# Kernel optimization log

Measured on AMD Instinct MI355X. Metric: run time of the kernel, lower is better.

## Reference

```python
import jax, jax.numpy as jnp
import numpy as np

K_SIZE = 3
STRIDE = 1
PAD = 1


def _extract_patches(X, k, stride, pad):
    """X: [N,H,W,C] -> patches [N,Ho,Wo,k*k*C], ordered (dh, dw, c) to match
    filters.reshape(c_out, k*k*C)."""
    Xp = jnp.pad(X, ((0, 0), (pad, pad), (pad, pad), (0, 0)))
    N, Hp, Wp, C = Xp.shape
    Ho = (Hp - k) // stride + 1
    Wo = (Wp - k) // stride + 1
    slabs = [Xp[:, dh:dh + stride * Ho:stride, dw:dw + stride * Wo:stride, :]
             for dh in range(k) for dw in range(k)]  # fixed small k*k loop
    P = jnp.stack(slabs, axis=3)  # [N,Ho,Wo,k*k,C]
    return P.reshape(N, Ho, Wo, k * k * C)


def setup_inputs() -> dict:
    key = jax.random.key(0)
    k1, k2 = jax.random.split(key)
    X = jax.random.normal(k1, (8, 32, 32, 32), dtype=jnp.float32)
    filters = jax.random.normal(k2, (64, 3, 3, 32), dtype=jnp.float32)
    return {"X": X, "filters": filters}


def reference(X, filters):
    # AdderNet forward: Z[n,h,w,f] = sum_{dh,dw,c} |window(n,h,w) - filters[f]|
    c_out = filters.shape[0]
    P = _extract_patches(X, K_SIZE, STRIDE, PAD)  # [N,Ho,Wo,K]
    N, Ho, Wo, K = P.shape
    F = filters.reshape(c_out, K)
    # L1 distance between every patch and every filter: [M, c_out]
    D = jnp.abs(P.reshape(-1, 1, K) - F[None, :, :]).sum(axis=-1)
    return D.reshape(N, Ho, Wo, c_out)
```

## Files before the change

### kernel.cpp

```cpp
#include <hip/hip_runtime.h>


#define BLOCK 256

__global__ __launch_bounds__(256, 2) void adder_fwd(const float* __restrict__ X,
                                                    const float* __restrict__ Fg,
                                                    float* __restrict__ out) {
    __shared__ float Xs[4 * 34 * 36];

    const int b = blockIdx.x;
    const int fq = b & 3;
    const int hp = (b >> 2) & 15;
    const int n = b >> 6;
    const int h0 = hp * 2;
    const int tid = threadIdx.x;

    #pragma unroll
    for (int i = 0; i < 5; ++i) {
        int idx = tid + BLOCK * i;
        if (idx < 1088) {
            int c4 = idx & 7;
            int t  = idx >> 3;
            int wc = t % 34;
            int rr = t / 34;
            int hr = h0 + rr - 1;
            int gw = wc - 1;
            float4 v = make_float4(0.f, 0.f, 0.f, 0.f);
            if ((unsigned)hr < 32u && (unsigned)gw < 32u) {
                v = ((const float4*)(X + (((size_t)n * 32 + hr) * 32 + gw) * 32))[c4];
            }
            ((float4*)(Xs + (rr * 34 + wc) * 36))[c4] = v;
        }
    }
    __syncthreads();

    const int w    = tid & 31;
    const int hh   = (tid >> 5) & 1;
    const int wave = __builtin_amdgcn_readfirstlane(tid >> 6);
    const int f0   = fq * 16 + wave * 4;

    const float* fb = Fg + (size_t)f0 * 288;

    float a0 = 0.f, a1 = 0.f, a2 = 0.f, a3 = 0.f;

    #pragma unroll
    for (int r = 0; r < 3; ++r) {
        #pragma unroll
        for (int dw = 0; dw < 3; ++dw) {
            const float4* xp = (const float4*)(Xs + ((hh + r) * 34 + (w + dw)) * 36);
            const float*  ftap = fb + (r * 3 + dw) * 32;
            #pragma unroll
            for (int c4 = 0; c4 < 8; ++c4) {
                float4 xv = xp[c4];
                float4 f0v = ((const float4*)(ftap + 0 * 288))[c4];
                float4 f1v = ((const float4*)(ftap + 1 * 288))[c4];
                float4 f2v = ((const float4*)(ftap + 2 * 288))[c4];
                float4 f3v = ((const float4*)(ftap + 3 * 288))[c4];
                a0 += fabsf(xv.x - f0v.x) + fabsf(xv.y - f0v.y)
                    + fabsf(xv.z - f0v.z) + fabsf(xv.w - f0v.w);
                a1 += fabsf(xv.x - f1v.x) + fabsf(xv.y - f1v.y)
                    + fabsf(xv.z - f1v.z) + fabsf(xv.w - f1v.w);
                a2 += fabsf(xv.x - f2v.x) + fabsf(xv.y - f2v.y)
                    + fabsf(xv.z - f2v.z) + fabsf(xv.w - f2v.w);
                a3 += fabsf(xv.x - f3v.x) + fabsf(xv.y - f3v.y)
                    + fabsf(xv.z - f3v.z) + fabsf(xv.w - f3v.w);
            }
        }
    }

    float4* o4 = (float4*)out;
    o4[(((size_t)n * 32 + h0 + hh) * 32 + w) * 16 + (f0 >> 2)] =
        make_float4(a0, a1, a2, a3);
}

extern "C" void kernel_launch(void* const* d_in, const int* in_sizes, int n_in,
                              void* d_out, int out_size, void* d_ws, size_t ws_size,
                              hipStream_t stream) {
    const float* X = (const float*)d_in[0];
    const float* F = (const float*)d_in[1];
    float* out = (float*)d_out;
    adder_fwd<<<dim3(512), dim3(256), 0, stream>>>(X, F, out);
}
```

Measured before the change: 69.17 us.

## Keep filters in registers, split channels across lanes, and reuse LDS input windows

```diff
diff --git a/kernel.cpp b/kernel.cpp
--- a/kernel.cpp
+++ b/kernel.cpp
@@ -3,74 +3,103 @@
 
 #define BLOCK 256
 
-__global__ __launch_bounds__(256, 2) void adder_fwd(const float* __restrict__ X,
+__global__ __launch_bounds__(256, 4) void adder_fwd(const float* __restrict__ X,
                                                     const float* __restrict__ Fg,
                                                     float* __restrict__ out) {
-    __shared__ float Xs[4 * 34 * 36];
+    __shared__ float Xs[3 * 18 * 32];
 
-    const int b = blockIdx.x;
-    const int fq = b & 3;
-    const int hp = (b >> 2) & 15;
-    const int n = b >> 6;
-    const int h0 = hp * 2;
+    const int b  = blockIdx.x;
+    const int fh = b & 1;
+    const int wh = (b >> 1) & 1;
+    const int h  = (b >> 2) & 31;
+    const int n  = b >> 7;
+    const int w0 = wh * 16;
     const int tid = threadIdx.x;
 
+    const int lane = tid & 63;
+    const int c8   = lane & 7;
+    const int f    = lane >> 3;
+    const int wave = __builtin_amdgcn_readfirstlane(tid >> 6);
+    const int f0   = fh * 32 + wave * 8;
+    const int fid  = f0 + f;
+
+    float4 fr[9];
+    {
+        const float* fp = Fg + (size_t)fid * 288 + c8 * 4;
+        #pragma unroll
+        for (int t = 0; t < 9; ++t)
+            fr[t] = *(const float4*)(fp + t * 32);
+    }
+
     #pragma unroll
-    for (int i = 0; i < 5; ++i) {
-        int idx = tid + BLOCK * i;
-        if (idx < 1088) {
-            int c4 = idx & 7;
-            int t  = idx >> 3;
-            int wc = t % 34;
-            int rr = t / 34;
-            int hr = h0 + rr - 1;
-            int gw = wc - 1;
+    for (int it = 0; it < 2; ++it) {
+        int idx = tid + BLOCK * it;
+        if (idx < 432) {
+            int c4  = idx & 7;
+            int t   = idx >> 3;
+            int col = t % 18;
+            int row = t / 18;
+            int hr  = h + row - 1;
+            int gw  = w0 + col - 1;
             float4 v = make_float4(0.f, 0.f, 0.f, 0.f);
-            if ((unsigned)hr < 32u && (unsigned)gw < 32u) {
+            if ((unsigned)hr < 32u && (unsigned)gw < 32u)
                 v = ((const float4*)(X + (((size_t)n * 32 + hr) * 32 + gw) * 32))[c4];
-            }
-            ((float4*)(Xs + (rr * 34 + wc) * 36))[c4] = v;
+            ((float4*)(Xs + (row * 18 + col) * 32))[c4] = v;
         }
     }
     __syncthreads();
 
-    const int w    = tid & 31;
-    const int hh   = (tid >> 5) & 1;
-    const int wave = __builtin_amdgcn_readfirstlane(tid >> 6);
-    const int f0   = fq * 16 + wave * 4;
+    const float* xb = Xs + c8 * 4;
+    const size_t obase = (((size_t)n * 32 + h) * 32 + w0) * 64 + fid;
 
-    const float* fb = Fg + (size_t)f0 * 288;
+    #pragma unroll 1
+    for (int pg = 0; pg < 4; ++pg) {
+        float4 acc[4];
+        #pragma unroll
+        for (int pp = 0; pp < 4; ++pp)
+            acc[pp] = make_float4(0.f, 0.f, 0.f, 0.f);
 
-    float a0 = 0.f, a1 = 0.f, a2 = 0.f, a3 = 0.f;
+        #pragma unroll
+        for (int dh = 0; dh < 3; ++dh) {
+            float4 x[6];
+            #pragma unroll
+            for (int j = 0; j < 6; ++j)
+                x[j] = *(const float4*)(xb + (dh * 18 + pg * 4 + j) * 32);
 
-    #pragma unroll
-    for (int r = 0; r < 3; ++r) {
-        #pragma unroll
-        for (int dw = 0; dw < 3; ++dw) {
-            const float4* xp = (const float4*)(Xs + ((hh + r) * 34 + (w + dw)) * 36);
-            const float*  ftap = fb + (r * 3 + dw) * 32;
             #pragma unroll
-            for (int c4 = 0; c4 < 8; ++c4) {
-                float4 xv = xp[c4];
-                float4 f0v = ((const float4*)(ftap + 0 * 288))[c4];
-                float4 f1v = ((const float4*)(ftap + 1 * 288))[c4];
-                float4 f2v = ((const float4*)(ftap + 2 * 288))[c4];
-                float4 f3v = ((const float4*)(ftap + 3 * 288))[c4];
-                a0 += fabsf(xv.x - f0v.x) + fabsf(xv.y - f0v.y)
-                    + fabsf(xv.z - f0v.z) + fabsf(xv.w - f0v.w);
-                a1 += fabsf(xv.x - f1v.x) + fabsf(xv.y - f1v.y)
-                    + fabsf(xv.z - f1v.z) + fabsf(xv.w - f1v.w);
-                a2 += fabsf(xv.x - f2v.x) + fabsf(xv.y - f2v.y)
-                    + fabsf(xv.z - f2v.z) + fabsf(xv.w - f2v.w);
-                a3 += fabsf(xv.x - f3v.x) + fabsf(xv.y - f3v.y)
-                    + fabsf(xv.z - f3v.z) + fabsf(xv.w - f3v.w);
+            for (int dw = 0; dw < 3; ++dw) {
+                const float4 fv = fr[dh * 3 + dw];
+                #pragma unroll
+                for (int pp = 0; pp < 4; ++pp) {
+                    const float4 xv = x[pp + dw];
+                    acc[pp].x += fabsf(xv.x - fv.x);
+                    acc[pp].y += fabsf(xv.y - fv.y);
+                    acc[pp].z += fabsf(xv.z - fv.z);
+                    acc[pp].w += fabsf(xv.w - fv.w);
+                }
             }
         }
+
+        float s0 = (acc[0].x + acc[0].y) + (acc[0].z + acc[0].w);
+        float s1 = (acc[1].x + acc[1].y) + (acc[1].z + acc[1].w);
+        float s2 = (acc[2].x + acc[2].y) + (acc[2].z + acc[2].w);
+        float s3 = (acc[3].x + acc[3].y) + (acc[3].z + acc[3].w);
+
+        s0 += __shfl_xor(s0, 1, 64);  s1 += __shfl_xor(s1, 1, 64);
+        s2 += __shfl_xor(s2, 1, 64);  s3 += __shfl_xor(s3, 1, 64);
+        s0 += __shfl_xor(s0, 2, 64);  s1 += __shfl_xor(s1, 2, 64);
+        s2 += __shfl_xor(s2, 2, 64);  s3 += __shfl_xor(s3, 2, 64);
+        s0 += __shfl_xor(s0, 4, 64);  s1 += __shfl_xor(s1, 4, 64);
+        s2 += __shfl_xor(s2, 4, 64);  s3 += __shfl_xor(s3, 4, 64);
+
+        if (c8 < 4) {
+            float v = s0;
+            if (c8 == 1) v = s1;
+            else if (c8 == 2) v = s2;
+            else if (c8 == 3) v = s3;
+            out[obase + (size_t)(pg * 4 + c8) * 64] = v;
+        }
     }
-
-    float4* o4 = (float4*)out;
-    o4[(((size_t)n * 32 + h0 + hh) * 32 + w) * 16 + (f0 >> 2)] =
-        make_float4(a0, a1, a2, a3);
 }
 
 extern "C" void kernel_launch(void* const* d_in, const int* in_sizes, int n_in,
@@ -79,5 +108,5 @@
     const float* X = (const float*)d_in[0];
     const float* F = (const float*)d_in[1];
     float* out = (float*)d_out;
-    adder_fwd<<<dim3(512), dim3(256), 0, stream>>>(X, F, out);
+    adder_fwd<<<dim3(1024), dim3(256), 0, stream>>>(X, F, out);
 }
```

Result: faster. 63.73 us (-7.9%).
